# Kernel optimization log

Measured on AMD Instinct MI355X. Metric: run time of the kernel, lower is better.

## Reference

```python
import jax, jax.numpy as jnp
import numpy as np

H = 512      # hidden_size (hardcoded in module)
WD = 1024    # word_dim (hardcoded)
V = 30000    # vocab/output size (len(picketdata)+4 stand-in)
B = 64
S = 256      # encoder sequence length
T = 28       # target sequence length


def setup_inputs() -> dict:
    key = jax.random.key(0)
    ks = jax.random.split(key, 20)
    p = lambda k, shp: (jax.random.normal(k, shp, dtype=jnp.float32) * 0.02)
    return {
        "encoder_last_hidden_state": jax.random.normal(ks[0], (1, B, H), dtype=jnp.float32),
        "encoder_output": jax.random.normal(ks[1], (B, S, H), dtype=jnp.float32),
        "targets": jax.random.randint(ks[2], (B, T), 0, V),
        "tr_steps": 100,
        "emb": p(ks[3], (V, WD)),
        # Attention MLP (note: no nonlinearities between linears, faithful to source)
        "W1": p(ks[4], (2 * H, H)), "b1": jnp.zeros((H,), jnp.float32),
        "W2": p(ks[5], (H, H)),     "b2": jnp.zeros((H,), jnp.float32),
        "W3": p(ks[6], (H, H)),     "b3": jnp.zeros((H,), jnp.float32),
        "Wv": p(ks[7], (H,)),  # to_weight, no bias
        # LSTM (input = H + WD = 1536), gate order i,f,g,o like torch
        "Wih": p(ks[8], (H + WD, 4 * H)),
        "Whh": p(ks[9], (H, 4 * H)),
        "bih": jnp.zeros((4 * H,), jnp.float32),
        "bhh": jnp.zeros((4 * H,), jnp.float32),
        # final output projection
        "Wout": p(ks[10], (H, V)), "bout": jnp.zeros((V,), jnp.float32),
    }


def reference(encoder_last_hidden_state, encoder_output, targets, tr_steps,
              emb, W1, b1, W2, b2, W3, b3, Wv, Wih, Whh, bih, bhh, Wout, bout):
    # threshold = expit(tr_steps/20 + 0.85) ~= 0.997 > uniform(0.05, 0.995)
    # -> the decoder ALWAYS feeds back its own argmax prediction (else-branch).
    seq_len = targets.shape[1]
    h0 = encoder_last_hidden_state[0]            # [B, H]
    c0 = jnp.zeros_like(h0)
    ciw0 = jnp.ones((h0.shape[0],), jnp.int32)   # <BOS>=1

    def step(carry, _):
        h, c, ciw = carry
        w = emb[ciw]                                             # [B, WD]
        # Attention over encoder outputs
        hs = jnp.broadcast_to(h[:, None, :], encoder_output.shape)
        m = jnp.concatenate([encoder_output, hs], axis=-1)       # [B, S, 2H]
        x = ((m @ W1 + b1) @ W2 + b2) @ W3 + b3                  # [B, S, H]
        aw = jax.nn.softmax(x @ Wv, axis=1)                      # [B, S]
        ctx = jnp.einsum('bs,bsh->bh', aw, encoder_output)       # [B, H]
        # LSTM cell
        xin = jnp.concatenate([w, ctx], axis=-1)                 # [B, WD+H]
        g = xin @ Wih + h @ Whh + bih + bhh                      # [B, 4H]
        i_, f_, g_, o_ = jnp.split(g, 4, axis=-1)
        c = jax.nn.sigmoid(f_) * c + jax.nn.sigmoid(i_) * jnp.tanh(g_)
        h = jax.nn.sigmoid(o_) * jnp.tanh(c)
        logits = h @ Wout + bout                                 # [B, V]
        ciw = jnp.argmax(logits, axis=-1).astype(jnp.int32)
        return (h, c, ciw), logits

    _, seq = jax.lax.scan(step, (h0, c0, ciw0), None, length=seq_len - 1)
    seq = jnp.transpose(seq, (1, 0, 2))                          # [B, T-1, V]
    seq_predictions = jnp.argmax(seq, axis=-1)                   # [B, T-1]
    return seq, seq_predictions
```

## Files before the change

kernel.cpp:

```cpp
#include <hip/hip_runtime.h>
#include <cstdint>
#include <cstddef>

static constexpr int H     = 512;
static constexpr int WD    = 1024;
static constexpr int NV    = 30000;
static constexpr int NB    = 64;
static constexpr int NS    = 256;
static constexpr int NSTEP = 27;
static constexpr int G4    = 2048;
static constexpr int NVT   = 1875;
static constexpr int PSTR  = 16;
static constexpr int NKT   = 48;

typedef __attribute__((ext_vector_type(8))) short  bf16x8;
typedef __attribute__((ext_vector_type(4))) float  f32x4;
typedef __attribute__((ext_vector_type(8))) unsigned short u16x8;

__device__ __forceinline__ unsigned fkey(float f) {
  unsigned u = __float_as_uint(f);
  return u ^ (0x80000000u | (unsigned)((int)u >> 31));
}

__device__ __forceinline__ unsigned short bf16rne(float f) {
  unsigned u = __float_as_uint(f);
  return (unsigned short)((u + 0x7FFFu + ((u >> 16) & 1u)) >> 16);
}

__global__ __launch_bounds__(512) void k_ue(
    const float* __restrict__ W1, const float* __restrict__ W2,
    const float* __restrict__ W3, const float* __restrict__ Wv,
    float* __restrict__ ue) {
  __shared__ float wv[H], t1[H], t2[H];
  const int tid = threadIdx.x;
  wv[tid] = Wv[tid];
  __syncthreads();
  {
    const float4* row = (const float4*)(W3 + (size_t)tid * H);
    float a = 0.f;
#pragma unroll 4
    for (int j = 0; j < H / 4; ++j) {
      float4 w = row[j];
      a += w.x * wv[4 * j] + w.y * wv[4 * j + 1] + w.z * wv[4 * j + 2] + w.w * wv[4 * j + 3];
    }
    t1[tid] = a;
  }
  __syncthreads();
  {
    const float4* row = (const float4*)(W2 + (size_t)tid * H);
    float a = 0.f;
#pragma unroll 4
    for (int j = 0; j < H / 4; ++j) {
      float4 w = row[j];
      a += w.x * t1[4 * j] + w.y * t1[4 * j + 1] + w.z * t1[4 * j + 2] + w.w * t1[4 * j + 3];
    }
    t2[tid] = a;
  }
  __syncthreads();
  {
    const float4* row = (const float4*)(W1 + (size_t)tid * H);
    float a = 0.f;
#pragma unroll 4
    for (int j = 0; j < H / 4; ++j) {
      float4 w = row[j];
      a += w.x * t2[4 * j] + w.y * t2[4 * j + 1] + w.z * t2[4 * j + 2] + w.w * t2[4 * j + 3];
    }
    ue[tid] = a;
  }
}

__global__ __launch_bounds__(256) void k_attn(
    const float* __restrict__ enc, const float* __restrict__ ue,
    float* __restrict__ ctx) {
  __shared__ float uel[H];
  __shared__ float sc[NS];
  __shared__ float red[NS];
  const int b = blockIdx.x;
  const int tid = threadIdx.x;
  uel[tid] = ue[tid];
  uel[tid + 256] = ue[tid + 256];
  __syncthreads();
  float acc = 0.f;
  {
    const float4* row = (const float4*)(enc + ((size_t)b * NS + tid) * H);
#pragma unroll 4
    for (int j = 0; j < H / 4; ++j) {
      float4 e = row[j];
      acc += e.x * uel[4 * j] + e.y * uel[4 * j + 1] + e.z * uel[4 * j + 2] + e.w * uel[4 * j + 3];
    }
  }
  red[tid] = acc;
  __syncthreads();
  for (int s = 128; s > 0; s >>= 1) {
    if (tid < s) red[tid] = fmaxf(red[tid], red[tid + s]);
    __syncthreads();
  }
  const float mx = red[0];
  __syncthreads();
  const float ex = expf(acc - mx);
  red[tid] = ex;
  __syncthreads();
  for (int s = 128; s > 0; s >>= 1) {
    if (tid < s) red[tid] += red[tid + s];
    __syncthreads();
  }
  const float inv = 1.f / red[0];
  sc[tid] = ex * inv;
  __syncthreads();
  for (int h0 = 0; h0 < H; h0 += 256) {
    const int hh = h0 + tid;
    float a = 0.f;
    for (int s = 0; s < NS; ++s) a += sc[s] * enc[((size_t)b * NS + s) * H + hh];
    ctx[b * H + hh] = a;
  }
}

__global__ __launch_bounds__(256) void k_gctx(
    const float* __restrict__ Wih, const float* __restrict__ bih,
    const float* __restrict__ bhh, const float* __restrict__ ctx,
    float* __restrict__ gctx) {
  __shared__ float cl[8 * H];
  const int tid = threadIdx.x;
  const int kx = blockIdx.x & 7, bg = blockIdx.x >> 3;
  const int k = kx * 256 + tid;
  for (int i = tid; i < 8 * H; i += 256) cl[i] = ctx[(size_t)bg * 8 * H + i];
  __syncthreads();
  float acc[8];
  const float bias = bih[k] + bhh[k];
#pragma unroll
  for (int r = 0; r < 8; ++r) acc[r] = bias;
  const float* wp = Wih + (size_t)WD * G4 + k;
  for (int j = 0; j < H; ++j) {
    float w = wp[(size_t)j * G4];
#pragma unroll
    for (int r = 0; r < 8; ++r) acc[r] += cl[r * H + j] * w;
  }
#pragma unroll
  for (int r = 0; r < 8; ++r) gctx[(size_t)(bg * 8 + r) * G4 + k] = acc[r];
}

__global__ __launch_bounds__(256) void k_convW(
    const float* __restrict__ Wout, unsigned short* __restrict__ whi,
    unsigned short* __restrict__ wlo) {
  const int gid = blockIdx.x * 256 + threadIdx.x;
  const int frag = gid >> 6, lane = gid & 63;
  const int vt = frag >> 4, kt = frag & 15;
  const int v  = vt * 16 + (lane & 15);
  const int k0 = kt * 32 + (lane >> 4) * 8;
  u16x8 hv, lv;
#pragma unroll
  for (int e = 0; e < 8; ++e) {
    float x = Wout[(size_t)(k0 + e) * NV + v];
    unsigned short hb = bf16rne(x);
    float hf = __uint_as_float((unsigned)hb << 16);
    hv[e] = hb;
    lv[e] = bf16rne(x - hf);
  }
  *(u16x8*)(whi + (size_t)gid * 8) = hv;
  *(u16x8*)(wlo + (size_t)gid * 8) = lv;
}

__global__ __launch_bounds__(256) void k_convW2(
    const float* __restrict__ Wih, const float* __restrict__ Whh,
    unsigned short* __restrict__ whi2, unsigned short* __restrict__ wlo2) {
  const int gid = blockIdx.x * 256 + threadIdx.x;
  const int frag = gid >> 6, lane = gid & 63;
  const int vt = frag / NKT, kt = frag % NKT;
  const int n  = vt * 16 + (lane & 15);
  const int k0 = kt * 32 + (lane >> 4) * 8;
  u16x8 hv, lv;
#pragma unroll
  for (int e = 0; e < 8; ++e) {
    int k = k0 + e;
    float x = (k < WD) ? Wih[(size_t)k * G4 + n] : Whh[(size_t)(k - WD) * G4 + n];
    unsigned short hb = bf16rne(x);
    float hf = __uint_as_float((unsigned)hb << 16);
    hv[e] = hb;
    lv[e] = bf16rne(x - hf);
  }
  *(u16x8*)(whi2 + (size_t)gid * 8) = hv;
  *(u16x8*)(wlo2 + (size_t)gid * 8) = lv;
}

__global__ __launch_bounds__(128) void k_emb(
    const float* __restrict__ emb, const float* __restrict__ encLast,
    const unsigned long long* __restrict__ packedPrev,
    unsigned long long* __restrict__ packedCur,
    float* __restrict__ pred,
    unsigned short* __restrict__ efhi, unsigned short* __restrict__ eflo,
    unsigned short* __restrict__ h0hi, unsigned short* __restrict__ h0lo,
    int step) {
  const int b = blockIdx.x, tid = threadIdx.x;
  int ciw = 1;
  if (step > 0) {
    unsigned long long kp = packedPrev[b * PSTR];
    ciw = 0x7FFFFFFF - (int)(unsigned)(kp & 0xFFFFFFFFull);
  }
  if (b == 0 && tid < NB) {
    if (step > 0) {
      unsigned long long kp = packedPrev[tid * PSTR];
      int v = 0x7FFFFFFF - (int)(unsigned)(kp & 0xFFFFFFFFull);
      pred[tid * NSTEP + (step - 1)] = (float)v;
    }
    packedCur[tid * PSTR] = 0ull;
  }
  const int mt = b >> 4;
  const int lane = (b & 15) | ((tid & 3) << 4);
  {
    const float* src = emb + (size_t)ciw * WD + tid * 8;
    float4 f0 = *(const float4*)src;
    float4 f1 = *(const float4*)(src + 4);
    float vals[8] = {f0.x, f0.y, f0.z, f0.w, f1.x, f1.y, f1.z, f1.w};
    u16x8 hv, lv;
#pragma unroll
    for (int e = 0; e < 8; ++e) {
      unsigned short hb = bf16rne(vals[e]);
      float hf = __uint_as_float((unsigned)hb << 16);
      hv[e] = hb;
      lv[e] = bf16rne(vals[e] - hf);
    }
    const size_t fi = ((size_t)(mt * 32 + (tid >> 2)) * 64 + lane) * 8;
    *(u16x8*)(efhi + fi) = hv;
    *(u16x8*)(eflo + fi) = lv;
  }
  if (step == 0 && tid < 64) {
    const float* src = encLast + (size_t)b * H + tid * 8;
    float4 f0 = *(const float4*)src;
    float4 f1 = *(const float4*)(src + 4);
    float vals[8] = {f0.x, f0.y, f0.z, f0.w, f1.x, f1.y, f1.z, f1.w};
    u16x8 hv, lv;
#pragma unroll
    for (int e = 0; e < 8; ++e) {
      unsigned short hb = bf16rne(vals[e]);
      float hf = __uint_as_float((unsigned)hb << 16);
      hv[e] = hb;
      lv[e] = bf16rne(vals[e] - hf);
    }
    const size_t fi = ((size_t)(mt * 16 + (tid >> 2)) * 64 + lane) * 8;
    *(u16x8*)(h0hi + fi) = hv;
    *(u16x8*)(h0lo + fi) = lv;
  }
}

__global__ __launch_bounds__(256) void k_gates(
    const unsigned short* __restrict__ whi2, const unsigned short* __restrict__ wlo2,
    const unsigned short* __restrict__ efhi, const unsigned short* __restrict__ eflo,
    const unsigned short* __restrict__ hihi, const unsigned short* __restrict__ hilo,
    unsigned short* __restrict__ hohi, unsigned short* __restrict__ holo,
    const float* __restrict__ gctx, float* __restrict__ cbuf, int step) {
  __shared__ float gl[4][32][17];
  const int tid = threadIdx.x;
  const int lane = tid & 63, g = tid >> 6;
  const int x = blockIdx.x, p = blockIdx.y;
  const int vt = g * 32 + x;

  f32x4 acc0 = {0.f, 0.f, 0.f, 0.f};
  f32x4 acc1 = {0.f, 0.f, 0.f, 0.f};
  const bf16x8* wh = (const bf16x8*)whi2 + (size_t)vt * NKT * 64 + lane;
  const bf16x8* wl = (const bf16x8*)wlo2 + (size_t)vt * NKT * 64 + lane;
  const bf16x8* aeh = (const bf16x8*)efhi + (size_t)(p * 2) * 32 * 64 + lane;
  const bf16x8* ael = (const bf16x8*)eflo + (size_t)(p * 2) * 32 * 64 + lane;
  const bf16x8* ahh = (const bf16x8*)hihi + (size_t)(p * 2) * 16 * 64 + lane;
  const bf16x8* ahl = (const bf16x8*)hilo + (size_t)(p * 2) * 16 * 64 + lane;
#pragma unroll 4
  for (int kt = 0; kt < 32; ++kt) {
    bf16x8 bh = wh[kt * 64];
    bf16x8 bl = wl[kt * 64];
    bf16x8 a0h = aeh[kt * 64];
    bf16x8 a0l = ael[kt * 64];
    bf16x8 a1h = aeh[(32 + kt) * 64];
    bf16x8 a1l = ael[(32 + kt) * 64];
    acc0 = __builtin_amdgcn_mfma_f32_16x16x32_bf16(a0h, bh, acc0, 0, 0, 0);
    acc0 = __builtin_amdgcn_mfma_f32_16x16x32_bf16(a0l, bh, acc0, 0, 0, 0);
    acc0 = __builtin_amdgcn_mfma_f32_16x16x32_bf16(a0h, bl, acc0, 0, 0, 0);
    acc1 = __builtin_amdgcn_mfma_f32_16x16x32_bf16(a1h, bh, acc1, 0, 0, 0);
    acc1 = __builtin_amdgcn_mfma_f32_16x16x32_bf16(a1l, bh, acc1, 0, 0, 0);
    acc1 = __builtin_amdgcn_mfma_f32_16x16x32_bf16(a1h, bl, acc1, 0, 0, 0);
  }
#pragma unroll 4
  for (int kt = 0; kt < 16; ++kt) {
    bf16x8 bh = wh[(32 + kt) * 64];
    bf16x8 bl = wl[(32 + kt) * 64];
    bf16x8 a0h = ahh[kt * 64];
    bf16x8 a0l = ahl[kt * 64];
    bf16x8 a1h = ahh[(16 + kt) * 64];
    bf16x8 a1l = ahl[(16 + kt) * 64];
    acc0 = __builtin_amdgcn_mfma_f32_16x16x32_bf16(a0h, bh, acc0, 0, 0, 0);
    acc0 = __builtin_amdgcn_mfma_f32_16x16x32_bf16(a0l, bh, acc0, 0, 0, 0);
    acc0 = __builtin_amdgcn_mfma_f32_16x16x32_bf16(a0h, bl, acc0, 0, 0, 0);
    acc1 = __builtin_amdgcn_mfma_f32_16x16x32_bf16(a1h, bh, acc1, 0, 0, 0);
    acc1 = __builtin_amdgcn_mfma_f32_16x16x32_bf16(a1l, bh, acc1, 0, 0, 0);
    acc1 = __builtin_amdgcn_mfma_f32_16x16x32_bf16(a1h, bl, acc1, 0, 0, 0);
  }
  {
    const int c = lane & 15, rbase = (lane >> 4) * 4;
#pragma unroll
    for (int r = 0; r < 4; ++r) {
      gl[g][rbase + r][c] = acc0[r];
      gl[g][16 + rbase + r][c] = acc1[r];
    }
  }
  __syncthreads();
  for (int pi = tid; pi < 512; pi += 256) {
    const int bl_ = pi >> 4, c = pi & 15;
    const int b = p * 32 + bl_;
    const int i = x * 16 + c;
    const float* gb = gctx + (size_t)b * G4 + i;
    float gi = gl[0][bl_][c] + gb[0];
    float gf = gl[1][bl_][c] + gb[512];
    float gg = gl[2][bl_][c] + gb[1024];
    float go = gl[3][bl_][c] + gb[1536];
    float cp = (step == 0) ? 0.f : cbuf[b * H + i];
    float si = 1.f / (1.f + expf(-gi));
    float sf = 1.f / (1.f + expf(-gf));
    float so = 1.f / (1.f + expf(-go));
    float cn = sf * cp + si * tanhf(gg);
    float hn = so * tanhf(cn);
    cbuf[b * H + i] = cn;
    unsigned short hb = bf16rne(hn);
    float hf = __uint_as_float((unsigned)hb << 16);
    unsigned short lb = bf16rne(hn - hf);
    const int mt = b >> 4;
    const int kt2 = i >> 5;
    const int lane2 = (b & 15) | (((i >> 3) & 3) << 4);
    const int e2 = i & 7;
    const size_t fi = ((size_t)(mt * 16 + kt2) * 64 + lane2) * 8 + e2;
    hohi[fi] = hb;
    holo[fi] = lb;
  }
}

__global__ __launch_bounds__(256) void k_logits_mfma(
    const unsigned short* __restrict__ whi, const unsigned short* __restrict__ wlo,
    const unsigned short* __restrict__ hfhi, const unsigned short* __restrict__ hflo,
    const float* __restrict__ bout, float* __restrict__ outSeq,
    unsigned long long* __restrict__ packedCur, int step) {
  const int tid  = threadIdx.x;
  const int lane = tid & 63;
  const int mt   = tid >> 6;
  const int vt0  = blockIdx.x * 4;
  const int vlane = lane & 15, rgrp = lane >> 4;

  bf16x8 ahi[16], alo[16];
  {
    const bf16x8* hh = (const bf16x8*)hfhi + (size_t)mt * 16 * 64 + lane;
    const bf16x8* hl = (const bf16x8*)hflo + (size_t)mt * 16 * 64 + lane;
#pragma unroll
    for (int kt = 0; kt < 16; ++kt) {
      ahi[kt] = hh[kt * 64];
      alo[kt] = hl[kt * 64];
    }
  }

  unsigned long long bestk[4] = {0ull, 0ull, 0ull, 0ull};

  for (int vv = 0; vv < 4; ++vv) {
    const int vt = vt0 + vv;
    if (vt >= NVT) break;
    f32x4 acc = {0.f, 0.f, 0.f, 0.f};
    const bf16x8* wh = (const bf16x8*)whi + (size_t)vt * 16 * 64 + lane;
    const bf16x8* wl = (const bf16x8*)wlo + (size_t)vt * 16 * 64 + lane;
#pragma unroll
    for (int kt = 0; kt < 16; ++kt) {
      bf16x8 bh = wh[kt * 64];
      bf16x8 bl = wl[kt * 64];
      acc = __builtin_amdgcn_mfma_f32_16x16x32_bf16(ahi[kt], bh, acc, 0, 0, 0);
      acc = __builtin_amdgcn_mfma_f32_16x16x32_bf16(alo[kt], bh, acc, 0, 0, 0);
      acc = __builtin_amdgcn_mfma_f32_16x16x32_bf16(ahi[kt], bl, acc, 0, 0, 0);
    }
    const int v = vt * 16 + vlane;
    const float bo = bout[v];
    const int bbase = mt * 16 + rgrp * 4;
    float* op = outSeq + ((size_t)bbase * NSTEP + step) * NV + v;
#pragma unroll
    for (int r = 0; r < 4; ++r) {
      float val = acc[r] + bo;
      op[(size_t)r * NSTEP * NV] = val;
      unsigned long long key = ((unsigned long long)fkey(val) << 32)
                             | (unsigned long long)(0x7FFFFFFFu - (unsigned)v);
      if (key > bestk[r]) bestk[r] = key;
    }
  }

#pragma unroll
  for (int m = 8; m >= 1; m >>= 1) {
#pragma unroll
    for (int r = 0; r < 4; ++r) {
      unsigned long long o = __shfl_xor(bestk[r], m, 64);
      if (o > bestk[r]) bestk[r] = o;
    }
  }
  if (vlane == 0) {
#pragma unroll
    for (int r = 0; r < 4; ++r)
      atomicMax(&packedCur[(mt * 16 + rgrp * 4 + r) * PSTR], bestk[r]);
  }
}

__global__ void k_predfinal(const unsigned long long* __restrict__ packed,
                            float* __restrict__ pred) {
  const int b = threadIdx.x;
  int v = 0x7FFFFFFF - (int)(unsigned)(packed[b * PSTR] & 0xFFFFFFFFull);
  pred[b * NSTEP + (NSTEP - 1)] = (float)v;
}

extern "C" void kernel_launch(void* const* d_in, const int* in_sizes, int n_in,
                              void* d_out, int out_size, void* d_ws, size_t ws_size,
                              hipStream_t stream) {
  (void)in_sizes; (void)n_in; (void)out_size; (void)ws_size;
  const float* encLast = (const float*)d_in[0];
  const float* enc     = (const float*)d_in[1];
  const float* emb     = (const float*)d_in[4];
  const float* W1      = (const float*)d_in[5];
  const float* W2      = (const float*)d_in[7];
  const float* W3      = (const float*)d_in[9];
  const float* Wv      = (const float*)d_in[11];
  const float* Wih     = (const float*)d_in[12];
  const float* Whh     = (const float*)d_in[13];
  const float* bih     = (const float*)d_in[14];
  const float* bhh     = (const float*)d_in[15];
  const float* Wout    = (const float*)d_in[16];
  const float* bout    = (const float*)d_in[17];

  float* wsf = (float*)d_ws;
  float* ue   = wsf;
  float* ctx  = wsf + 512;
  float* gctx = wsf + 33280;
  float* cbuf = wsf + 164352;
  unsigned long long* packedP = (unsigned long long*)(wsf + 197120);
  unsigned short* efhi = (unsigned short*)(wsf + 252416);
  unsigned short* eflo = (unsigned short*)(wsf + 285184);
  unsigned short* h0hi = (unsigned short*)(wsf + 317952);
  unsigned short* h0lo = (unsigned short*)(wsf + 334336);
  unsigned short* h1hi = (unsigned short*)(wsf + 350720);
  unsigned short* h1lo = (unsigned short*)(wsf + 367104);
  unsigned short* whi2 = (unsigned short*)(wsf + 383488);
  unsigned short* wlo2 = (unsigned short*)(wsf + 1956352);
  unsigned short* whi  = (unsigned short*)(wsf + 3529216);
  unsigned short* wlo  = (unsigned short*)(wsf + 11209216);

  float* outSeq = (float*)d_out;
  float* pred   = outSeq + (size_t)NB * NSTEP * NV;

  k_ue    <<<1, 512, 0, stream>>>(W1, W2, W3, Wv, ue);
  k_attn  <<<NB, 256, 0, stream>>>(enc, ue, ctx);
  k_gctx  <<<64, 256, 0, stream>>>(Wih, bih, bhh, ctx, gctx);
  k_convW <<<7500, 256, 0, stream>>>(Wout, whi, wlo);
  k_convW2<<<1536, 256, 0, stream>>>(Wih, Whh, whi2, wlo2);

  for (int t = 0; t < NSTEP; ++t) {
    const unsigned long long* pprev = packedP + (t > 0 ? (size_t)(t - 1) * NB * PSTR : 0);
    unsigned long long* pcur = packedP + (size_t)t * NB * PSTR;
    const unsigned short* hihi = (t & 1) ? h1hi : h0hi;
    const unsigned short* hilo = (t & 1) ? h1lo : h0lo;
    unsigned short* hohi = (t & 1) ? h0hi : h1hi;
    unsigned short* holo = (t & 1) ? h0lo : h1lo;
    k_emb<<<NB, 128, 0, stream>>>(emb, encLast, pprev, pcur, pred,
                                  efhi, eflo, h0hi, h0lo, t);
    k_gates<<<dim3(32, 2), 256, 0, stream>>>(whi2, wlo2, efhi, eflo,
                                             hihi, hilo, hohi, holo,
                                             gctx, cbuf, t);
    k_logits_mfma<<<469, 256, 0, stream>>>(whi, wlo, hohi, holo, bout, outSeq,
                                           pcur, t);
  }
  k_predfinal<<<1, NB, 0, stream>>>(packedP + (size_t)(NSTEP - 1) * NB * PSTR, pred);
}
```

Measured before the change: 2.065 ms.

## Fuse embedding gather into gates kernel, split K across warps, retile logits

Drops the per-step embedding kernel. The gates kernel now reads the argmax token ids, gathers the embedding rows and splits them into bf16 hi/lo parts inline, and it splits the K loop across two warp groups (512 threads) whose partial sums are reduced in shared memory. The initial hidden-state conversion moves to a one-time kernel. The logits kernel now handles two vocab tiles per block with twice as many blocks, streaming A fragments instead of holding 16 in registers, which aims at more parallelism and occupancy. This removes one launch and a global round trip per step, at the cost of redundant embedding splitting across blocks.

```diff
diff --git a/kernel.cpp b/kernel.cpp
--- a/kernel.cpp
+++ b/kernel.cpp
@@ -27,6 +27,16 @@
   return (unsigned short)((u + 0x7FFFu + ((u >> 16) & 1u)) >> 16);
 }
 
+__device__ __forceinline__ void split8(float4 f0, float4 f1, bf16x8& hi, bf16x8& lo) {
+  float v[8] = {f0.x, f0.y, f0.z, f0.w, f1.x, f1.y, f1.z, f1.w};
+#pragma unroll
+  for (int e = 0; e < 8; ++e) {
+    unsigned short hb = bf16rne(v[e]);
+    hi[e] = (short)hb;
+    lo[e] = (short)bf16rne(v[e] - __uint_as_float((unsigned)hb << 16));
+  }
+}
+
 __global__ __launch_bounds__(512) void k_ue(
     const float* __restrict__ W1, const float* __restrict__ W2,
     const float* __restrict__ W3, const float* __restrict__ Wv,
@@ -182,21 +192,47 @@
   *(u16x8*)(wlo2 + (size_t)gid * 8) = lv;
 }
 
-__global__ __launch_bounds__(128) void k_emb(
-    const float* __restrict__ emb, const float* __restrict__ encLast,
+__global__ __launch_bounds__(64) void k_h0(
+    const float* __restrict__ encLast,
+    unsigned short* __restrict__ h0hi, unsigned short* __restrict__ h0lo) {
+  const int b = blockIdx.x, tid = threadIdx.x;
+  const int mt = b >> 4;
+  const int lane = (b & 15) | ((tid & 3) << 4);
+  const float* src = encLast + (size_t)b * H + tid * 8;
+  bf16x8 hv, lv;
+  split8(*(const float4*)src, *(const float4*)(src + 4), hv, lv);
+  const size_t fi = ((size_t)(mt * 16 + (tid >> 2)) * 64 + lane) * 8;
+  *(bf16x8*)(h0hi + fi) = hv;
+  *(bf16x8*)(h0lo + fi) = lv;
+}
+
+__global__ __launch_bounds__(512) void k_gates(
+    const unsigned short* __restrict__ whi2, const unsigned short* __restrict__ wlo2,
+    const float* __restrict__ emb,
+    const unsigned short* __restrict__ hihi, const unsigned short* __restrict__ hilo,
+    unsigned short* __restrict__ hohi, unsigned short* __restrict__ holo,
     const unsigned long long* __restrict__ packedPrev,
     unsigned long long* __restrict__ packedCur,
     float* __restrict__ pred,
-    unsigned short* __restrict__ efhi, unsigned short* __restrict__ eflo,
-    unsigned short* __restrict__ h0hi, unsigned short* __restrict__ h0lo,
-    int step) {
-  const int b = blockIdx.x, tid = threadIdx.x;
-  int ciw = 1;
-  if (step > 0) {
-    unsigned long long kp = packedPrev[b * PSTR];
-    ciw = 0x7FFFFFFF - (int)(unsigned)(kp & 0xFFFFFFFFull);
-  }
-  if (b == 0 && tid < NB) {
+    const float* __restrict__ gctx, float* __restrict__ cbuf, int step) {
+  __shared__ float gl[8][32][17];
+  __shared__ int ciws[32];
+  const int tid = threadIdx.x;
+  const int lane = tid & 63, w = tid >> 6;
+  const int g = w & 3, kh = w >> 2;
+  const int x = blockIdx.x, p = blockIdx.y;
+  const int vt = g * 32 + x;
+
+  if (tid < 32) {
+    int b = p * 32 + tid;
+    int ciw = 1;
+    if (step > 0) {
+      unsigned long long kp = packedPrev[b * PSTR];
+      ciw = 0x7FFFFFFF - (int)(unsigned)(kp & 0xFFFFFFFFull);
+    }
+    ciws[tid] = ciw;
+  }
+  if (x == 0 && p == 0 && tid < NB) {
     if (step > 0) {
       unsigned long long kp = packedPrev[tid * PSTR];
       int v = 0x7FFFFFFF - (int)(unsigned)(kp & 0xFFFFFFFFull);
@@ -204,72 +240,35 @@
     }
     packedCur[tid * PSTR] = 0ull;
   }
-  const int mt = b >> 4;
-  const int lane = (b & 15) | ((tid & 3) << 4);
-  {
-    const float* src = emb + (size_t)ciw * WD + tid * 8;
-    float4 f0 = *(const float4*)src;
-    float4 f1 = *(const float4*)(src + 4);
-    float vals[8] = {f0.x, f0.y, f0.z, f0.w, f1.x, f1.y, f1.z, f1.w};
-    u16x8 hv, lv;
-#pragma unroll
-    for (int e = 0; e < 8; ++e) {
-      unsigned short hb = bf16rne(vals[e]);
-      float hf = __uint_as_float((unsigned)hb << 16);
-      hv[e] = hb;
-      lv[e] = bf16rne(vals[e] - hf);
-    }
-    const size_t fi = ((size_t)(mt * 32 + (tid >> 2)) * 64 + lane) * 8;
-    *(u16x8*)(efhi + fi) = hv;
-    *(u16x8*)(eflo + fi) = lv;
-  }
-  if (step == 0 && tid < 64) {
-    const float* src = encLast + (size_t)b * H + tid * 8;
-    float4 f0 = *(const float4*)src;
-    float4 f1 = *(const float4*)(src + 4);
-    float vals[8] = {f0.x, f0.y, f0.z, f0.w, f1.x, f1.y, f1.z, f1.w};
-    u16x8 hv, lv;
-#pragma unroll
-    for (int e = 0; e < 8; ++e) {
-      unsigned short hb = bf16rne(vals[e]);
-      float hf = __uint_as_float((unsigned)hb << 16);
-      hv[e] = hb;
-      lv[e] = bf16rne(vals[e] - hf);
-    }
-    const size_t fi = ((size_t)(mt * 16 + (tid >> 2)) * 64 + lane) * 8;
-    *(u16x8*)(h0hi + fi) = hv;
-    *(u16x8*)(h0lo + fi) = lv;
-  }
-}
-
-__global__ __launch_bounds__(256) void k_gates(
-    const unsigned short* __restrict__ whi2, const unsigned short* __restrict__ wlo2,
-    const unsigned short* __restrict__ efhi, const unsigned short* __restrict__ eflo,
-    const unsigned short* __restrict__ hihi, const unsigned short* __restrict__ hilo,
-    unsigned short* __restrict__ hohi, unsigned short* __restrict__ holo,
-    const float* __restrict__ gctx, float* __restrict__ cbuf, int step) {
-  __shared__ float gl[4][32][17];
-  const int tid = threadIdx.x;
-  const int lane = tid & 63, g = tid >> 6;
-  const int x = blockIdx.x, p = blockIdx.y;
-  const int vt = g * 32 + x;
+  __syncthreads();
+
+  const float* rb0 = emb + (size_t)ciws[lane & 15] * WD;
+  const float* rb1 = emb + (size_t)ciws[16 + (lane & 15)] * WD;
+  const int koff = (lane >> 4) * 8;
 
   f32x4 acc0 = {0.f, 0.f, 0.f, 0.f};
   f32x4 acc1 = {0.f, 0.f, 0.f, 0.f};
   const bf16x8* wh = (const bf16x8*)whi2 + (size_t)vt * NKT * 64 + lane;
   const bf16x8* wl = (const bf16x8*)wlo2 + (size_t)vt * NKT * 64 + lane;
-  const bf16x8* aeh = (const bf16x8*)efhi + (size_t)(p * 2) * 32 * 64 + lane;
-  const bf16x8* ael = (const bf16x8*)eflo + (size_t)(p * 2) * 32 * 64 + lane;
   const bf16x8* ahh = (const bf16x8*)hihi + (size_t)(p * 2) * 16 * 64 + lane;
   const bf16x8* ahl = (const bf16x8*)hilo + (size_t)(p * 2) * 16 * 64 + lane;
-#pragma unroll 4
-  for (int kt = 0; kt < 32; ++kt) {
+
+  const int kt0 = kh * 24;
+#pragma unroll 2
+  for (int kt = kt0; kt < kt0 + 24; ++kt) {
     bf16x8 bh = wh[kt * 64];
     bf16x8 bl = wl[kt * 64];
-    bf16x8 a0h = aeh[kt * 64];
-    bf16x8 a0l = ael[kt * 64];
-    bf16x8 a1h = aeh[(32 + kt) * 64];
-    bf16x8 a1l = ael[(32 + kt) * 64];
+    bf16x8 a0h, a0l, a1h, a1l;
+    if (kt < 32) {
+      const float* s0 = rb0 + kt * 32 + koff;
+      const float* s1 = rb1 + kt * 32 + koff;
+      split8(*(const float4*)s0, *(const float4*)(s0 + 4), a0h, a0l);
+      split8(*(const float4*)s1, *(const float4*)(s1 + 4), a1h, a1l);
+    } else {
+      const int ht = kt - 32;
+      a0h = ahh[ht * 64];        a0l = ahl[ht * 64];
+      a1h = ahh[(16 + ht) * 64]; a1l = ahl[(16 + ht) * 64];
+    }
     acc0 = __builtin_amdgcn_mfma_f32_16x16x32_bf16(a0h, bh, acc0, 0, 0, 0);
     acc0 = __builtin_amdgcn_mfma_f32_16x16x32_bf16(a0l, bh, acc0, 0, 0, 0);
     acc0 = __builtin_amdgcn_mfma_f32_16x16x32_bf16(a0h, bl, acc0, 0, 0, 0);
@@ -277,39 +276,24 @@
     acc1 = __builtin_amdgcn_mfma_f32_16x16x32_bf16(a1l, bh, acc1, 0, 0, 0);
     acc1 = __builtin_amdgcn_mfma_f32_16x16x32_bf16(a1h, bl, acc1, 0, 0, 0);
   }
-#pragma unroll 4
-  for (int kt = 0; kt < 16; ++kt) {
-    bf16x8 bh = wh[(32 + kt) * 64];
-    bf16x8 bl = wl[(32 + kt) * 64];
-    bf16x8 a0h = ahh[kt * 64];
-    bf16x8 a0l = ahl[kt * 64];
-    bf16x8 a1h = ahh[(16 + kt) * 64];
-    bf16x8 a1l = ahl[(16 + kt) * 64];
-    acc0 = __builtin_amdgcn_mfma_f32_16x16x32_bf16(a0h, bh, acc0, 0, 0, 0);
-    acc0 = __builtin_amdgcn_mfma_f32_16x16x32_bf16(a0l, bh, acc0, 0, 0, 0);
-    acc0 = __builtin_amdgcn_mfma_f32_16x16x32_bf16(a0h, bl, acc0, 0, 0, 0);
-    acc1 = __builtin_amdgcn_mfma_f32_16x16x32_bf16(a1h, bh, acc1, 0, 0, 0);
-    acc1 = __builtin_amdgcn_mfma_f32_16x16x32_bf16(a1l, bh, acc1, 0, 0, 0);
-    acc1 = __builtin_amdgcn_mfma_f32_16x16x32_bf16(a1h, bl, acc1, 0, 0, 0);
-  }
   {
     const int c = lane & 15, rbase = (lane >> 4) * 4;
 #pragma unroll
     for (int r = 0; r < 4; ++r) {
-      gl[g][rbase + r][c] = acc0[r];
-      gl[g][16 + rbase + r][c] = acc1[r];
-    }
-  }
-  __syncthreads();
-  for (int pi = tid; pi < 512; pi += 256) {
-    const int bl_ = pi >> 4, c = pi & 15;
+      gl[w][rbase + r][c] = acc0[r];
+      gl[w][16 + rbase + r][c] = acc1[r];
+    }
+  }
+  __syncthreads();
+  {
+    const int bl_ = tid >> 4, c = tid & 15;
     const int b = p * 32 + bl_;
     const int i = x * 16 + c;
     const float* gb = gctx + (size_t)b * G4 + i;
-    float gi = gl[0][bl_][c] + gb[0];
-    float gf = gl[1][bl_][c] + gb[512];
-    float gg = gl[2][bl_][c] + gb[1024];
-    float go = gl[3][bl_][c] + gb[1536];
+    float gi = gl[0][bl_][c] + gl[4][bl_][c] + gb[0];
+    float gf = gl[1][bl_][c] + gl[5][bl_][c] + gb[512];
+    float gg = gl[2][bl_][c] + gl[6][bl_][c] + gb[1024];
+    float go = gl[3][bl_][c] + gl[7][bl_][c] + gb[1536];
     float cp = (step == 0) ? 0.f : cbuf[b * H + i];
     float si = 1.f / (1.f + expf(-gi));
     float sf = 1.f / (1.f + expf(-gf));
@@ -330,7 +314,7 @@
   }
 }
 
-__global__ __launch_bounds__(256) void k_logits_mfma(
+__global__ __launch_bounds__(256, 4) void k_logits_mfma(
     const unsigned short* __restrict__ whi, const unsigned short* __restrict__ wlo,
     const unsigned short* __restrict__ hfhi, const unsigned short* __restrict__ hflo,
     const float* __restrict__ bout, float* __restrict__ outSeq,
@@ -338,49 +322,64 @@
   const int tid  = threadIdx.x;
   const int lane = tid & 63;
   const int mt   = tid >> 6;
-  const int vt0  = blockIdx.x * 4;
+  const int vtA  = blockIdx.x * 2;
+  const bool vbok = (vtA + 1) < NVT;
+  const int vtB  = vbok ? vtA + 1 : vtA;
   const int vlane = lane & 15, rgrp = lane >> 4;
 
-  bf16x8 ahi[16], alo[16];
-  {
-    const bf16x8* hh = (const bf16x8*)hfhi + (size_t)mt * 16 * 64 + lane;
-    const bf16x8* hl = (const bf16x8*)hflo + (size_t)mt * 16 * 64 + lane;
-#pragma unroll
-    for (int kt = 0; kt < 16; ++kt) {
-      ahi[kt] = hh[kt * 64];
-      alo[kt] = hl[kt * 64];
-    }
+  const bf16x8* hh  = (const bf16x8*)hfhi + (size_t)mt * 16 * 64 + lane;
+  const bf16x8* hl  = (const bf16x8*)hflo + (size_t)mt * 16 * 64 + lane;
+  const bf16x8* whA = (const bf16x8*)whi + (size_t)vtA * 16 * 64 + lane;
+  const bf16x8* wlA = (const bf16x8*)wlo + (size_t)vtA * 16 * 64 + lane;
+  const bf16x8* whB = (const bf16x8*)whi + (size_t)vtB * 16 * 64 + lane;
+  const bf16x8* wlB = (const bf16x8*)wlo + (size_t)vtB * 16 * 64 + lane;
+
+  f32x4 accA = {0.f, 0.f, 0.f, 0.f};
+  f32x4 accB = {0.f, 0.f, 0.f, 0.f};
+#pragma unroll 2
+  for (int kt = 0; kt < 16; ++kt) {
+    bf16x8 ah = hh[kt * 64];
+    bf16x8 al = hl[kt * 64];
+    bf16x8 bhA = whA[kt * 64];
+    bf16x8 blA = wlA[kt * 64];
+    bf16x8 bhB = whB[kt * 64];
+    bf16x8 blB = wlB[kt * 64];
+    accA = __builtin_amdgcn_mfma_f32_16x16x32_bf16(ah, bhA, accA, 0, 0, 0);
+    accA = __builtin_amdgcn_mfma_f32_16x16x32_bf16(al, bhA, accA, 0, 0, 0);
+    accA = __builtin_amdgcn_mfma_f32_16x16x32_bf16(ah, blA, accA, 0, 0, 0);
+    accB = __builtin_amdgcn_mfma_f32_16x16x32_bf16(ah, bhB, accB, 0, 0, 0);
+    accB = __builtin_amdgcn_mfma_f32_16x16x32_bf16(al, bhB, accB, 0, 0, 0);
+    accB = __builtin_amdgcn_mfma_f32_16x16x32_bf16(ah, blB, accB, 0, 0, 0);
   }
 
   unsigned long long bestk[4] = {0ull, 0ull, 0ull, 0ull};
-
-  for (int vv = 0; vv < 4; ++vv) {
-    const int vt = vt0 + vv;
-    if (vt >= NVT) break;
-    f32x4 acc = {0.f, 0.f, 0.f, 0.f};
-    const bf16x8* wh = (const bf16x8*)whi + (size_t)vt * 16 * 64 + lane;
-    const bf16x8* wl = (const bf16x8*)wlo + (size_t)vt * 16 * 64 + lane;
-#pragma unroll
-    for (int kt = 0; kt < 16; ++kt) {
-      bf16x8 bh = wh[kt * 64];
-      bf16x8 bl = wl[kt * 64];
-      acc = __builtin_amdgcn_mfma_f32_16x16x32_bf16(ahi[kt], bh, acc, 0, 0, 0);
-      acc = __builtin_amdgcn_mfma_f32_16x16x32_bf16(alo[kt], bh, acc, 0, 0, 0);
-      acc = __builtin_amdgcn_mfma_f32_16x16x32_bf16(ahi[kt], bl, acc, 0, 0, 0);
-    }
-    const int v = vt * 16 + vlane;
+  const int bbase = mt * 16 + rgrp * 4;
+  {
+    const int v = vtA * 16 + vlane;
     const float bo = bout[v];
-    const int bbase = mt * 16 + rgrp * 4;
     float* op = outSeq + ((size_t)bbase * NSTEP + step) * NV + v;
 #pragma unroll
     for (int r = 0; r < 4; ++r) {
-      float val = acc[r] + bo;
+      float val = accA[r] + bo;
       op[(size_t)r * NSTEP * NV] = val;
       unsigned long long key = ((unsigned long long)fkey(val) << 32)
                              | (unsigned long long)(0x7FFFFFFFu - (unsigned)v);
       if (key > bestk[r]) bestk[r] = key;
     }
   }
+  if (vbok) {
+    const int v = vtB * 16 + vlane;
+    const float bo = bout[v];
+    float* op = outSeq + ((size_t)bbase * NSTEP + step) * NV + v;
+#pragma unroll
+    for (int r = 0; r < 4; ++r) {
+      float val = accB[r] + bo;
+      op[(size_t)r * NSTEP * NV] = val;
+      unsigned long long key = ((unsigned long long)fkey(val) << 32)
+                             | (unsigned long long)(0x7FFFFFFFu - (unsigned)v);
+      if (key > bestk[r]) bestk[r] = key;
+    }
+  }
 
 #pragma unroll
   for (int m = 8; m >= 1; m >>= 1) {
@@ -393,7 +392,7 @@
   if (vlane == 0) {
 #pragma unroll
     for (int r = 0; r < 4; ++r)
-      atomicMax(&packedCur[(mt * 16 + rgrp * 4 + r) * PSTR], bestk[r]);
+      atomicMax(&packedCur[(bbase + r) * PSTR], bestk[r]);
   }
 }
 
@@ -428,16 +427,14 @@
   float* gctx = wsf + 33280;
   float* cbuf = wsf + 164352;
   unsigned long long* packedP = (unsigned long long*)(wsf + 197120);
-  unsigned short* efhi = (unsigned short*)(wsf + 252416);
-  unsigned short* eflo = (unsigned short*)(wsf + 285184);
-  unsigned short* h0hi = (unsigned short*)(wsf + 317952);
-  unsigned short* h0lo = (unsigned short*)(wsf + 334336);
-  unsigned short* h1hi = (unsigned short*)(wsf + 350720);
-  unsigned short* h1lo = (unsigned short*)(wsf + 367104);
-  unsigned short* whi2 = (unsigned short*)(wsf + 383488);
-  unsigned short* wlo2 = (unsigned short*)(wsf + 1956352);
-  unsigned short* whi  = (unsigned short*)(wsf + 3529216);
-  unsigned short* wlo  = (unsigned short*)(wsf + 11209216);
+  unsigned short* h0hi = (unsigned short*)(wsf + 252416);
+  unsigned short* h0lo = (unsigned short*)(wsf + 268800);
+  unsigned short* h1hi = (unsigned short*)(wsf + 285184);
+  unsigned short* h1lo = (unsigned short*)(wsf + 301568);
+  unsigned short* whi2 = (unsigned short*)(wsf + 317952);
+  unsigned short* wlo2 = (unsigned short*)(wsf + 1890816);
+  unsigned short* whi  = (unsigned short*)(wsf + 3463680);
+  unsigned short* wlo  = (unsigned short*)(wsf + 11143680);
 
   float* outSeq = (float*)d_out;
   float* pred   = outSeq + (size_t)NB * NSTEP * NV;
@@ -447,6 +444,7 @@
   k_gctx  <<<64, 256, 0, stream>>>(Wih, bih, bhh, ctx, gctx);
   k_convW <<<7500, 256, 0, stream>>>(Wout, whi, wlo);
   k_convW2<<<1536, 256, 0, stream>>>(Wih, Whh, whi2, wlo2);
+  k_h0    <<<NB, 64, 0, stream>>>(encLast, h0hi, h0lo);
 
   for (int t = 0; t < NSTEP; ++t) {
     const unsigned long long* pprev = packedP + (t > 0 ? (size_t)(t - 1) * NB * PSTR : 0);
@@ -455,12 +453,11 @@
     const unsigned short* hilo = (t & 1) ? h1lo : h0lo;
     unsigned short* hohi = (t & 1) ? h0hi : h1hi;
     unsigned short* holo = (t & 1) ? h0lo : h1lo;
-    k_emb<<<NB, 128, 0, stream>>>(emb, encLast, pprev, pcur, pred,
-                                  efhi, eflo, h0hi, h0lo, t);
-    k_gates<<<dim3(32, 2), 256, 0, stream>>>(whi2, wlo2, efhi, eflo,
+    k_gates<<<dim3(32, 2), 512, 0, stream>>>(whi2, wlo2, emb,
                                              hihi, hilo, hohi, holo,
+                                             pprev, pcur, pred,
                                              gctx, cbuf, t);
-    k_logits_mfma<<<469, 256, 0, stream>>>(whi, wlo, hohi, holo, bout, outSeq,
+    k_logits_mfma<<<938, 256, 0, stream>>>(whi, wlo, hohi, holo, bout, outSeq,
                                            pcur, t);
   }
   k_predfinal<<<1, NB, 0, stream>>>(packedP + (size_t)(NSTEP - 1) * NB * PSTR, pred);
```

Result: faster. 1.794 ms (-13.1%).
